# Kernel tuning notes

Measured on AMD Instinct MI355X. Metric: run time of the kernel, lower is better.

## Reference

```python
import jax, jax.numpy as jnp
import numpy as np

B, A, N = 1024, 64, 256   # batch, n_agent, obs_shape
M = 128                    # thought_size
H = M // 2                 # bi-LSTM hidden per direction
ACT = 64                   # action_shape
E_ATT = 64                 # attention embedding
E1 = M                     # actor_1 embedding (defaults to thought_size)
E2 = M                     # actor_2 embedding
K = 8                      # agent_per_group
THRESH = 0.5
LN_EPS = 1e-5


def setup_inputs() -> dict:
    key = jax.random.key(0)
    ks = jax.random.split(key, 32)
    r = lambda k, shp, s=0.05: jax.random.normal(k, shp, jnp.float32) * s
    return {
        'obs': jax.random.normal(ks[0], (B, A, N), jnp.float32),
        # actor_1: Linear(N,E1) -> LayerNorm(E1) -> ReLU -> Linear(E1,M)
        'a1_w1': r(ks[1], (E1, N)), 'a1_b1': r(ks[2], (E1,)),
        'ln_g': jnp.ones((E1,), jnp.float32), 'ln_b': jnp.zeros((E1,), jnp.float32),
        'a1_w2': r(ks[3], (M, E1)), 'a1_b2': r(ks[4], (M,)),
        # attention unit: 3-layer MLP
        'att_w1': r(ks[5], (E_ATT, M)), 'att_b1': r(ks[6], (E_ATT,)),
        'att_w2': r(ks[7], (E_ATT, E_ATT)), 'att_b2': r(ks[8], (E_ATT,)),
        'att_w3': r(ks[9], (1, E_ATT)), 'att_b3': r(ks[10], (1,)),
        # bi-LSTM (torch gate order i,f,g,o), forward + backward directions
        'wih_f': r(ks[11], (4 * H, M)), 'whh_f': r(ks[12], (4 * H, H)),
        'bih_f': r(ks[13], (4 * H,)), 'bhh_f': r(ks[14], (4 * H,)),
        'wih_b': r(ks[15], (4 * H, M)), 'whh_b': r(ks[16], (4 * H, H)),
        'bih_b': r(ks[17], (4 * H,)), 'bhh_b': r(ks[18], (4 * H,)),
        # actor_2: ReLU -> Linear(2M,E2) -> Linear(E2,ACT,no bias) -> Tanh
        'a2_w1': r(ks[19], (E2, 2 * M)), 'a2_b1': r(ks[20], (E2,)),
        'a2_w2': r(ks[21], (ACT, E2)),
    }


def _lstm_dir(x, wih, whh, b):
    # x: (T, M) single sequence; returns (T, H)
    def cell(carry, xt):
        h, c = carry
        z = xt @ wih.T + h @ whh.T + b
        i, f, g, o = jnp.split(z, 4)
        c = jax.nn.sigmoid(f) * c + jax.nn.sigmoid(i) * jnp.tanh(g)
        h = jax.nn.sigmoid(o) * jnp.tanh(c)
        return (h, c), h
    init = (jnp.zeros((H,), x.dtype), jnp.zeros((H,), x.dtype))
    _, hs = jax.lax.scan(cell, init, x)
    return hs


def _bilstm(x, wih_f, whh_f, bf, wih_b, whh_b, bb):
    hf = _lstm_dir(x, wih_f, whh_f, bf)
    hb = _lstm_dir(x[::-1], wih_b, whh_b, bb)[::-1]
    return jnp.concatenate([hf, hb], axis=-1)  # (T, 2H) == (T, M)


def reference(obs, a1_w1, a1_b1, ln_g, ln_b, a1_w2, a1_b2,
              att_w1, att_b1, att_w2, att_b2, att_w3, att_b3,
              wih_f, whh_f, bih_f, bhh_f, wih_b, whh_b, bih_b, bhh_b,
              a2_w1, a2_b1, a2_w2):
    # ---- actor_1: obs -> thoughts ----
    h = obs @ a1_w1.T + a1_b1
    mu = h.mean(-1, keepdims=True)
    var = ((h - mu) ** 2).mean(-1, keepdims=True)
    h = (h - mu) * jax.lax.rsqrt(var + LN_EPS) * ln_g + ln_b
    thoughts = jax.nn.relu(h) @ a1_w2.T + a1_b2  # (B, A, M)

    # ---- attention unit: initiator probability ----
    a = jax.nn.relu(thoughts @ att_w1.T + att_b1)
    a = jax.nn.relu(a @ att_w2.T + att_b2)
    init_prob = jax.nn.sigmoid((a @ att_w3.T + att_b3)[..., 0])  # (B, A)
    is_init = init_prob > THRESH

    # ---- group formation: K nearest agents by squared distance ----
    dot = jnp.einsum('bim,bjm->bij', thoughts, thoughts)
    sq = jnp.einsum('bim,bim->bi', thoughts, thoughts)
    dists = sq[:, None, :] - 2.0 * dot + sq[:, :, None]  # (B, A, A)
    # torch scatters by ascending agent index (j-loop), so sort chosen indices
    idx = jnp.sort(jnp.argsort(dists, axis=-1)[..., :K], axis=-1)  # (B, A, K)

    # ---- sequential gather -> bi-LSTM -> scatter, per initiator in order ----
    bf, bb = bih_f + bhh_f, bih_b + bhh_b

    def update_one_batch(nt0, idx_b, init_b):
        def body(nt, inp):
            idx_i, init_i = inp
            gathered = nt[idx_i]                      # (K, M) from CURRENT state
            integ = _bilstm(gathered, wih_f, whh_f, bf, wih_b, whh_b, bb)
            upd = nt.at[idx_i].set(integ)
            return jnp.where(init_i, upd, nt), None
        nt, _ = jax.lax.scan(body, nt0, (idx_b, init_b))
        return nt

    new_thoughts = jax.vmap(update_one_batch)(thoughts, idx, is_init)  # (B, A, M)

    # ---- actor_2 ----
    x = jax.nn.relu(jnp.concatenate([thoughts, new_thoughts], axis=-1))
    x = x @ a2_w1.T + a2_b1
    action = jnp.tanh(x @ a2_w2.T)  # (B, A, ACT)
    return action


if __name__ == '__main__':
    out = reference(**setup_inputs())
    print(out.shape)
```

## Files before the change

### kernel.cpp

```cpp
#include <hip/hip_runtime.h>

typedef unsigned int u32;
typedef unsigned short u16;
typedef unsigned long long u64;
typedef _Float16 h2 __attribute__((ext_vector_type(2)));
typedef _Float16 h4 __attribute__((ext_vector_type(4)));
typedef _Float16 h8 __attribute__((ext_vector_type(8)));
typedef float f4 __attribute__((ext_vector_type(4)));

#define ROWS 65536
#define NB 1024
#define NA 64

__device__ __forceinline__ float dot4(float4 w, float4 x){
  return w.x*x.x + w.y*x.y + w.z*x.z + w.w*x.w;
}
__device__ __forceinline__ h2 u32_h2(u32 v){ union { u32 u; h2 h; } x; x.u = v; return x.h; }
__device__ __forceinline__ h2 pack_h2(float a, float b){ h2 r; r.x = (_Float16)a; r.y = (_Float16)b; return r; }
__device__ __forceinline__ h4 pack_h4(float4 v){
  h4 r; r.x=(_Float16)v.x; r.y=(_Float16)v.y; r.z=(_Float16)v.z; r.w=(_Float16)v.w; return r;
}
__device__ __forceinline__ h4 pack_h4_relu(float4 v){
  h4 r; r.x=(_Float16)fmaxf(v.x,0.f); r.y=(_Float16)fmaxf(v.y,0.f);
  r.z=(_Float16)fmaxf(v.z,0.f); r.w=(_Float16)fmaxf(v.w,0.f); return r;
}
__device__ __forceinline__ float fsig(float z){
  float e = __builtin_amdgcn_exp2f(-1.44269504f * z);
  return __builtin_amdgcn_rcpf(1.0f + e);
}
__device__ __forceinline__ float ftanh(float z){
  float e = __builtin_amdgcn_exp2f(2.885390082f * z);
  return 1.0f - 2.0f * __builtin_amdgcn_rcpf(1.0f + e);
}
__device__ __forceinline__ h8 load8f(const float* p){
  float4 a = *(const float4*)p;
  float4 b = *(const float4*)(p + 4);
  h8 r;
  r[0] = (_Float16)a.x; r[1] = (_Float16)a.y; r[2] = (_Float16)a.z; r[3] = (_Float16)a.w;
  r[4] = (_Float16)b.x; r[5] = (_Float16)b.y; r[6] = (_Float16)b.z; r[7] = (_Float16)b.w;
  return r;
}

__global__ __launch_bounds__(256) void k_cvt(
    const float* __restrict__ a2w1, const float* __restrict__ a2w2,
    _Float16* __restrict__ w1h, _Float16* __restrict__ w2h)
{
  int i = blockIdx.x * 256 + threadIdx.x;
  if (i < 32768) w1h[i] = (_Float16)a2w1[i];
  if (i < 8192)  w2h[i] = (_Float16)a2w2[i];
}

__global__ __launch_bounds__(128) void k_actor1(
    const float* __restrict__ obs, const float* __restrict__ w1, const float* __restrict__ b1,
    const float* __restrict__ lng, const float* __restrict__ lnb,
    const float* __restrict__ w2, const float* __restrict__ b2,
    const float* __restrict__ aw1, const float* __restrict__ ab1,
    const float* __restrict__ aw2, const float* __restrict__ ab2,
    const float* __restrict__ aw3, const float* __restrict__ ab3,
    float* __restrict__ thoughts, int* __restrict__ isinit)
{
  const int b0 = blockIdx.x * 8;
  const int t = threadIdx.x;
  __shared__ float4 xs[8][64];
  __shared__ float hs[8][128];
  __shared__ float tb[8][128];
  __shared__ float ab[8][64];
  __shared__ float a2b[8][64];
  __shared__ float red[8][4];

  { const float4* og = (const float4*)(obs + (size_t)b0 * 256);
    #pragma unroll
    for (int j = 0; j < 4; j++){ int p = j * 128 + t; xs[p >> 6][p & 63] = og[p]; } }
  __syncthreads();

  float acc[8];
  #pragma unroll
  for (int r = 0; r < 8; r++) acc[r] = b1[t];
  { const float4* wr = (const float4*)(w1 + (size_t)t * 256);
    for (int j = 0; j < 64; j++){
      float4 w = wr[j];
      #pragma unroll
      for (int r = 0; r < 8; r++) acc[r] += dot4(w, xs[r][j]);
    } }

  #pragma unroll
  for (int r = 0; r < 8; r++){
    float s = acc[r], s2 = acc[r] * acc[r];
    #pragma unroll
    for (int off = 32; off > 0; off >>= 1){ s += __shfl_down(s, off); s2 += __shfl_down(s2, off); }
    if ((t & 63) == 0){ red[r][t >> 6] = s; red[r][2 + (t >> 6)] = s2; }
  }
  __syncthreads();
  const float g_ = lng[t], bb_ = lnb[t];
  #pragma unroll
  for (int r = 0; r < 8; r++){
    float mu  = (red[r][0] + red[r][1]) * (1.0f/128.0f);
    float var = (red[r][2] + red[r][3]) * (1.0f/128.0f) - mu * mu;
    hs[r][t] = fmaxf((acc[r] - mu) * rsqrtf(var + 1e-5f) * g_ + bb_, 0.0f);
  }
  __syncthreads();

  float acc2[8];
  #pragma unroll
  for (int r = 0; r < 8; r++) acc2[r] = b2[t];
  { const float4* wr = (const float4*)(w2 + (size_t)t * 128);
    for (int j = 0; j < 32; j++){
      float4 w = wr[j];
      #pragma unroll
      for (int r = 0; r < 8; r++) acc2[r] += dot4(w, ((const float4*)hs[r])[j]);
    } }
  #pragma unroll
  for (int r = 0; r < 8; r++){
    thoughts[(size_t)(b0 + r) * 128 + t] = acc2[r];
    tb[r][t] = acc2[r];
  }
  __syncthreads();

  if (t < 64){
    float a[8];
    #pragma unroll
    for (int r = 0; r < 8; r++) a[r] = ab1[t];
    const float4* wr = (const float4*)(aw1 + (size_t)t * 128);
    for (int j = 0; j < 32; j++){
      float4 w = wr[j];
      #pragma unroll
      for (int r = 0; r < 8; r++) a[r] += dot4(w, ((const float4*)tb[r])[j]);
    }
    #pragma unroll
    for (int r = 0; r < 8; r++) ab[r][t] = fmaxf(a[r], 0.0f);
  }
  __syncthreads();
  if (t < 64){
    float a[8];
    #pragma unroll
    for (int r = 0; r < 8; r++) a[r] = ab2[t];
    const float4* wr = (const float4*)(aw2 + (size_t)t * 64);
    for (int j = 0; j < 16; j++){
      float4 w = wr[j];
      #pragma unroll
      for (int r = 0; r < 8; r++) a[r] += dot4(w, ((const float4*)ab[r])[j]);
    }
    #pragma unroll
    for (int r = 0; r < 8; r++) a2b[r][t] = fmaxf(a[r], 0.0f);
  }
  __syncthreads();
  if (t < 8){
    float p = ab3[0];
    for (int j = 0; j < 64; j++) p += aw3[j] * a2b[t][j];
    isinit[b0 + t] = (p > 0.0f) ? 1 : 0;
  }
}

__global__ __launch_bounds__(256) void k_groups(
    const float* __restrict__ thoughts, int* __restrict__ idxout)
{
  const int b = blockIdx.x;
  const int tid = threadIdx.x;
  __shared__ float T[64 * 130];
  __shared__ float sq[64];
  for (int p = tid; p < 8192; p += 256){
    T[(p >> 7) * 130 + (p & 127)] = thoughts[(size_t)b * 8192 + p];
  }
  __syncthreads();
  if (tid < 64){
    const float2* tj = (const float2*)&T[tid * 130];
    float s = 0.0f;
    #pragma unroll 8
    for (int k = 0; k < 64; k++){ float2 v = tj[k]; s += v.x*v.x + v.y*v.y; }
    sq[tid] = s;
  }
  __syncthreads();
  const int lane = tid & 63;
  const int wv = tid >> 6;
  const float2* tj = (const float2*)&T[lane * 130];
  const float sqj = sq[lane];
  for (int ii = 0; ii < 16; ii++){
    const int i = wv * 16 + ii;
    const float2* ti = (const float2*)&T[i * 130];
    float dot = 0.0f;
    #pragma unroll 8
    for (int k = 0; k < 64; k++){ float2 a = ti[k]; float2 c = tj[k]; dot += a.x*c.x + a.y*c.y; }
    float d = fmaxf(sq[i] + sqj - 2.0f*dot, 0.0f);
    u64 key = (((u64)__float_as_uint(d)) << 32) | (u32)lane;
    u64 mask = 0;
    for (int q = 0; q < 8; q++){
      u64 m = key;
      #pragma unroll
      for (int off = 32; off > 0; off >>= 1){ u64 o = __shfl_xor(m, off); if (o < m) m = o; }
      mask |= 1ull << (u32)(m & 63u);
      if (key == m) key = ~0ull;
    }
    if (lane == 0){
      u64 mm = mask;
      int base = (b * 64 + i) * 8;
      #pragma unroll
      for (int q = 0; q < 8; q++){ int j = (int)__builtin_ctzll(mm); mm &= mm - 1; idxout[base + q] = j; }
    }
  }
}

__global__ __launch_bounds__(512) void k_scan(
    const float* __restrict__ thoughts, const int* __restrict__ isinit, const int* __restrict__ idx,
    const float* __restrict__ wihf, const float* __restrict__ whhf,
    const float* __restrict__ bihf, const float* __restrict__ bhhf,
    const float* __restrict__ wihb, const float* __restrict__ whhb,
    const float* __restrict__ bihb, const float* __restrict__ bhhb,
    float* __restrict__ newt)
{
  const int b    = blockIdx.x;
  const int tid  = threadIdx.x;
  const int w    = tid >> 6;
  const int lane = tid & 63;
  const int dir  = w >> 2;
  const int wsub = w & 3;
  const int lr   = lane & 15;
  const int hi   = lane >> 4;

  __shared__ __align__(16) _Float16 nt16[64 * 136];
  __shared__ __align__(16) _Float16 Zx16[2*8*64*4];
  __shared__ __align__(16) _Float16 hb16[2][64];
  __shared__ int gall[512];
  __shared__ int flags[64];
  __shared__ int dirty[64];

  const float* wih = dir ? wihb : wihf;
  const float* whh = dir ? whhb : whhf;

  h8 Bf[4][4];
  #pragma unroll
  for (int ni = 0; ni < 4; ni++){
    const float* wr = wih + (size_t)((wsub << 6) + (ni << 4) + lr) * 128 + (hi << 3);
    #pragma unroll
    for (int kt = 0; kt < 4; kt++) Bf[ni][kt] = load8f(wr + kt * 32);
    __builtin_amdgcn_sched_barrier(0);
  }
  h8 Bh[4][2];
  #pragma unroll
  for (int gg = 0; gg < 4; gg++){
    const float* wr = whh + (size_t)((gg << 6) + (wsub << 4) + lr) * 64 + (hi << 3);
    #pragma unroll
    for (int kt = 0; kt < 2; kt++) Bh[gg][kt] = load8f(wr + kt * 32);
    __builtin_amdgcn_sched_barrier(0);
  }
  float biasl[4];
  {
    const float* bih = dir ? bihb : bihf;
    const float* bhh = dir ? bhhb : bhhf;
    #pragma unroll
    for (int ni = 0; ni < 4; ni++){
      int n = (wsub << 6) + (ni << 4) + lr;
      biasl[ni] = bih[n] + bhh[n];
    }
  }

  { const float4* tf4 = (const float4*)(thoughts + (size_t)b * 8192);
    #pragma unroll
    for (int k2 = 0; k2 < 4; k2++){
      int id4 = tid + k2 * 512;
      float4 v = tf4[id4];
      *(h4*)&nt16[(id4 >> 5) * 136 + (id4 & 31) * 4] = pack_h4(v);
    } }
  gall[tid] = idx[(size_t)b * 512 + tid];
  if (tid < 64){ flags[tid] = isinit[b * 64 + tid]; dirty[tid] = 0; }
  __syncthreads();

  #pragma unroll 1
  for (int i = 0; i < 64; i++){
    if (!flags[i]) continue;
    if (tid < 8) dirty[gall[i * 8 + tid]] = 1;
    const int grow = gall[i * 8 + (lr & 7)];

    {
      h8 Af[4];
      #pragma unroll
      for (int kt = 0; kt < 4; kt++)
        Af[kt] = *(const h8*)&nt16[grow * 136 + kt * 32 + (hi << 3)];
      #pragma unroll
      for (int ni = 0; ni < 4; ni++){
        f4 acc = {0.0f, 0.0f, 0.0f, 0.0f};
        #pragma unroll
        for (int kt = 0; kt < 4; kt++)
          acc = __builtin_amdgcn_mfma_f32_16x16x32_f16(Af[kt], Bf[ni][kt], acc, 0, 0, 0);
        if (lane < 32){
          const int t0 = hi << 2, lp = (ni << 4) + lr;
          #pragma unroll
          for (int r = 0; r < 4; r++)
            Zx16[(((dir << 3) + t0 + r) * 64 + lp) * 4 + wsub] = (_Float16)(acc[r] + biasl[ni]);
        }
      }
    }
    __syncthreads();

    float c = 0.0f;
    #pragma unroll
    for (int s = 0; s < 8; s++){
      const int tt = dir ? (7 - s) : s;
      uint2 zr = *(const uint2*)&Zx16[(((dir << 3) + tt) * 64 + (wsub << 4) + lr) * 4];
      h2 zlo = u32_h2(zr.x), zhi2 = u32_h2(zr.y);
      float z0 = (float)zlo.x, z1 = (float)zlo.y, z2 = (float)zhi2.x, z3 = (float)zhi2.y;
      if (s > 0){
        h8 a0 = *(const h8*)&hb16[dir][(hi << 3)];
        h8 a1 = *(const h8*)&hb16[dir][32 + (hi << 3)];
        f4 A0 = {z0, 0.0f, 0.0f, 0.0f};
        f4 A1 = {z1, 0.0f, 0.0f, 0.0f};
        f4 A2 = {z2, 0.0f, 0.0f, 0.0f};
        f4 A3 = {z3, 0.0f, 0.0f, 0.0f};
        A0 = __builtin_amdgcn_mfma_f32_16x16x32_f16(a0, Bh[0][0], A0, 0, 0, 0);
        A0 = __builtin_amdgcn_mfma_f32_16x16x32_f16(a1, Bh[0][1], A0, 0, 0, 0);
        A1 = __builtin_amdgcn_mfma_f32_16x16x32_f16(a0, Bh[1][0], A1, 0, 0, 0);
        A1 = __builtin_amdgcn_mfma_f32_16x16x32_f16(a1, Bh[1][1], A1, 0, 0, 0);
        A2 = __builtin_amdgcn_mfma_f32_16x16x32_f16(a0, Bh[2][0], A2, 0, 0, 0);
        A2 = __builtin_amdgcn_mfma_f32_16x16x32_f16(a1, Bh[2][1], A2, 0, 0, 0);
        A3 = __builtin_amdgcn_mfma_f32_16x16x32_f16(a0, Bh[3][0], A3, 0, 0, 0);
        A3 = __builtin_amdgcn_mfma_f32_16x16x32_f16(a1, Bh[3][1], A3, 0, 0, 0);
        z0 = A0[0]; z1 = A1[0]; z2 = A2[0]; z3 = A3[0];
      }
      float fi = fsig(z0);
      float ff = fsig(z1);
      float fg = ftanh(z2);
      float fo = fsig(z3);
      c = ff * c + fi * fg;
      float hn = fo * ftanh(c);
      if (hi == 0){
        hb16[dir][(wsub << 4) + lr] = (_Float16)hn;
        int gt = gall[i * 8 + tt];
        nt16[gt * 136 + (dir << 6) + (wsub << 4) + lr] = (_Float16)hn;
      }
      __syncthreads();
    }
  }

  __syncthreads();
  { const float4* tf4 = (const float4*)(thoughts + (size_t)b * 8192);
    float4* of4 = (float4*)(newt + (size_t)b * 8192);
    #pragma unroll
    for (int k2 = 0; k2 < 4; k2++){
      int id4 = tid + k2 * 512;
      int row = id4 >> 5, c4 = (id4 & 31) * 4;
      float4 v = tf4[id4];
      if (dirty[row]){
        h4 hv = *(const h4*)&nt16[row * 136 + c4];
        v.x = (float)hv.x; v.y = (float)hv.y; v.z = (float)hv.z; v.w = (float)hv.w;
      }
      of4[id4] = v;
    } }
}

__global__ __launch_bounds__(256) void k_actor2(
    const float* __restrict__ thoughts, const float* __restrict__ newt,
    const _Float16* __restrict__ w1h, const float* __restrict__ b1,
    const _Float16* __restrict__ w2h, float* __restrict__ out)
{
  const int b0 = blockIdx.x * 32;
  const int tid = threadIdx.x;
  const int w = tid >> 6, lane = tid & 63, lr = lane & 15, hi = lane >> 4;
  const int mt = w & 1, nb = (w >> 1) << 6;

  __shared__ __align__(16) _Float16 Xc[32 * 264];
  __shared__ __align__(16) _Float16 Ys[32 * 136];

  #pragma unroll
  for (int k2 = 0; k2 < 8; k2++){
    int id4 = tid + k2 * 256;
    int row = id4 >> 6, c4 = (id4 & 63) * 4;
    const float* src = (c4 < 128) ? (thoughts + (size_t)(b0 + row) * 128 + c4)
                                  : (newt + (size_t)(b0 + row) * 128 + (c4 - 128));
    float4 v = *(const float4*)src;
    *(h4*)&Xc[row * 264 + c4] = pack_h4_relu(v);
  }
  __syncthreads();

  {
    h8 Af[8];
    #pragma unroll
    for (int kt = 0; kt < 8; kt++)
      Af[kt] = *(const h8*)&Xc[(mt * 16 + lr) * 264 + kt * 32 + (hi << 3)];
    #pragma unroll
    for (int ni = 0; ni < 4; ni++){
      const int n = nb + ni * 16 + lr;
      const _Float16* wr = w1h + (size_t)n * 256 + (hi << 3);
      f4 acc = {0.0f, 0.0f, 0.0f, 0.0f};
      #pragma unroll
      for (int kt = 0; kt < 8; kt++){
        h8 bfr = *(const h8*)(wr + kt * 32);
        acc = __builtin_amdgcn_mfma_f32_16x16x32_f16(Af[kt], bfr, acc, 0, 0, 0);
      }
      const float bb = b1[n];
      #pragma unroll
      for (int r = 0; r < 4; r++){
        int row = mt * 16 + (hi << 2) + r;
        Ys[row * 136 + n] = (_Float16)(acc[r] + bb);
      }
    }
  }
  __syncthreads();

  {
    const int ni0 = (w >> 1) << 1;
    h8 Ag[4];
    #pragma unroll
    for (int kt = 0; kt < 4; kt++)
      Ag[kt] = *(const h8*)&Ys[(mt * 16 + lr) * 136 + kt * 32 + (hi << 3)];
    #pragma unroll
    for (int nj = 0; nj < 2; nj++){
      const int n = (ni0 + nj) * 16 + lr;
      const _Float16* wr = w2h + (size_t)n * 128 + (hi << 3);
      f4 acc = {0.0f, 0.0f, 0.0f, 0.0f};
      #pragma unroll
      for (int kt = 0; kt < 4; kt++){
        h8 bfr = *(const h8*)(wr + kt * 32);
        acc = __builtin_amdgcn_mfma_f32_16x16x32_f16(Ag[kt], bfr, acc, 0, 0, 0);
      }
      #pragma unroll
      for (int r = 0; r < 4; r++){
        int row = mt * 16 + (hi << 2) + r;
        out[(size_t)(b0 + row) * 64 + n] = ftanh(acc[r]);
      }
    }
  }
}

extern "C" void kernel_launch(void* const* d_in, const int* in_sizes, int n_in,
                              void* d_out, int out_size, void* d_ws, size_t ws_size,
                              hipStream_t stream)
{
  const float* obs  = (const float*)d_in[0];
  const float* w1   = (const float*)d_in[1];
  const float* b1   = (const float*)d_in[2];
  const float* lng  = (const float*)d_in[3];
  const float* lnb  = (const float*)d_in[4];
  const float* w2   = (const float*)d_in[5];
  const float* b2   = (const float*)d_in[6];
  const float* aw1  = (const float*)d_in[7];
  const float* ab1  = (const float*)d_in[8];
  const float* aw2  = (const float*)d_in[9];
  const float* ab2  = (const float*)d_in[10];
  const float* aw3  = (const float*)d_in[11];
  const float* ab3  = (const float*)d_in[12];
  const float* wihf = (const float*)d_in[13];
  const float* whhf = (const float*)d_in[14];
  const float* bihf = (const float*)d_in[15];
  const float* bhhf = (const float*)d_in[16];
  const float* wihb = (const float*)d_in[17];
  const float* whhb = (const float*)d_in[18];
  const float* bihb = (const float*)d_in[19];
  const float* bhhb = (const float*)d_in[20];
  const float* a2w1 = (const float*)d_in[21];
  const float* a2b1 = (const float*)d_in[22];
  const float* a2w2 = (const float*)d_in[23];

  float* thoughts = (float*)d_ws;
  float* newt     = thoughts + (size_t)ROWS * 128;
  int*   isinit   = (int*)(newt + (size_t)ROWS * 128);
  int*   idxb     = isinit + ROWS;
  _Float16* w1h   = (_Float16*)(idxb + (size_t)ROWS * 8);
  _Float16* w2h   = w1h + 32768;

  hipLaunchKernelGGL(k_cvt, dim3(128), dim3(256), 0, stream, a2w1, a2w2, w1h, w2h);
  hipLaunchKernelGGL(k_actor1, dim3(ROWS / 8), dim3(128), 0, stream,
                     obs, w1, b1, lng, lnb, w2, b2, aw1, ab1, aw2, ab2, aw3, ab3,
                     thoughts, isinit);
  hipLaunchKernelGGL(k_groups, dim3(NB), dim3(256), 0, stream, thoughts, idxb);
  hipLaunchKernelGGL(k_scan, dim3(NB), dim3(512), 0, stream,
                     thoughts, isinit, idxb,
                     wihf, whhf, bihf, bhhf, wihb, whhb, bihb, bhhb, newt);
  hipLaunchKernelGGL(k_actor2, dim3(ROWS / 32), dim3(256), 0, stream,
                     thoughts, newt, w1h, a2b1, w2h, (float*)d_out);
}
```

Baseline: 1.011 ms.

## Run LSTM recurrence in one wave per direction using bpermute instead of block barriers

Restructures the bi-LSTM scan kernel so one wave per direction owns the whole recurrent step. It keeps all of W_hh in registers and broadcasts the hidden state across lanes with ds_bpermute, which removes the per-timestep block-wide __syncthreads and the shared-memory hidden-state buffer. The other three waves per direction take over the input projection, spread over 16 column tiles. The price is serial work concentrated in one wave, with 32 MFMAs per step instead of 8 per wave, 16 bpermutes per step, and high register pressure from 32 h8 weight fragments.

```diff
diff --git a/kernel.cpp b/kernel.cpp
--- a/kernel.cpp
+++ b/kernel.cpp
@@ -39,6 +39,9 @@
   r[0] = (_Float16)a.x; r[1] = (_Float16)a.y; r[2] = (_Float16)a.z; r[3] = (_Float16)a.w;
   r[4] = (_Float16)b.x; r[5] = (_Float16)b.y; r[6] = (_Float16)b.z; r[7] = (_Float16)b.w;
   return r;
+}
+__device__ __forceinline__ float bperm_f(int addr, float v){
+  return __int_as_float(__builtin_amdgcn_ds_bpermute(addr, __float_as_int(v)));
 }
 
 __global__ __launch_bounds__(256) void k_cvt(
@@ -215,10 +218,10 @@
   const int wsub = w & 3;
   const int lr   = lane & 15;
   const int hi   = lane >> 4;
+  const bool isB = (wsub == 0);
 
   __shared__ __align__(16) _Float16 nt16[64 * 136];
   __shared__ __align__(16) _Float16 Zx16[2*8*64*4];
-  __shared__ __align__(16) _Float16 hb16[2][64];
   __shared__ int gall[512];
   __shared__ int flags[64];
   __shared__ int dirty[64];
@@ -226,30 +229,32 @@
   const float* wih = dir ? wihb : wihf;
   const float* whh = dir ? whhb : whhf;
 
-  h8 Bf[4][4];
-  #pragma unroll
-  for (int ni = 0; ni < 4; ni++){
-    const float* wr = wih + (size_t)((wsub << 6) + (ni << 4) + lr) * 128 + (hi << 3);
-    #pragma unroll
-    for (int kt = 0; kt < 4; kt++) Bf[ni][kt] = load8f(wr + kt * 32);
-    __builtin_amdgcn_sched_barrier(0);
-  }
-  h8 Bh[4][2];
-  #pragma unroll
-  for (int gg = 0; gg < 4; gg++){
-    const float* wr = whh + (size_t)((gg << 6) + (wsub << 4) + lr) * 64 + (hi << 3);
-    #pragma unroll
-    for (int kt = 0; kt < 2; kt++) Bh[gg][kt] = load8f(wr + kt * 32);
-    __builtin_amdgcn_sched_barrier(0);
-  }
-  float biasl[4];
-  {
+  h8 W[32];
+  float biasl[6];
+  if (isB){
+    #pragma unroll
+    for (int ct = 0; ct < 16; ct++){
+      const int n = ((ct >> 2) << 6) + ((ct & 3) << 4) + lr;
+      const float* wr = whh + (size_t)n * 64 + (hi << 3);
+      W[ct * 2 + 0] = load8f(wr);
+      W[ct * 2 + 1] = load8f(wr + 32);
+      __builtin_amdgcn_sched_barrier(0);
+    }
+  } else {
+    const int ai = wsub - 1;
     const float* bih = dir ? bihb : bihf;
     const float* bhh = dir ? bhhb : bhhf;
     #pragma unroll
-    for (int ni = 0; ni < 4; ni++){
-      int n = (wsub << 6) + (ni << 4) + lr;
-      biasl[ni] = bih[n] + bhh[n];
+    for (int k = 0; k < 6; k++){
+      const int ct = ai * 6 + k;
+      if (ct < 16){
+        const int n = ((ct >> 2) << 6) + ((ct & 3) << 4) + lr;
+        const float* wr = wih + (size_t)n * 128 + (hi << 3);
+        #pragma unroll
+        for (int kt = 0; kt < 4; kt++) W[k * 4 + kt] = load8f(wr + kt * 32);
+        biasl[k] = bih[n] + bhh[n];
+      }
+      __builtin_amdgcn_sched_barrier(0);
     }
   }
 
@@ -268,66 +273,84 @@
   for (int i = 0; i < 64; i++){
     if (!flags[i]) continue;
     if (tid < 8) dirty[gall[i * 8 + tid]] = 1;
-    const int grow = gall[i * 8 + (lr & 7)];
-
-    {
+
+    if (!isB){
+      const int ai = wsub - 1;
+      const int grow = gall[i * 8 + (lr & 7)];
       h8 Af[4];
       #pragma unroll
       for (int kt = 0; kt < 4; kt++)
         Af[kt] = *(const h8*)&nt16[grow * 136 + kt * 32 + (hi << 3)];
       #pragma unroll
-      for (int ni = 0; ni < 4; ni++){
-        f4 acc = {0.0f, 0.0f, 0.0f, 0.0f};
-        #pragma unroll
-        for (int kt = 0; kt < 4; kt++)
-          acc = __builtin_amdgcn_mfma_f32_16x16x32_f16(Af[kt], Bf[ni][kt], acc, 0, 0, 0);
-        if (lane < 32){
-          const int t0 = hi << 2, lp = (ni << 4) + lr;
+      for (int k = 0; k < 6; k++){
+        const int ct = ai * 6 + k;
+        if (ct < 16){
+          f4 acc = {0.0f, 0.0f, 0.0f, 0.0f};
           #pragma unroll
-          for (int r = 0; r < 4; r++)
-            Zx16[(((dir << 3) + t0 + r) * 64 + lp) * 4 + wsub] = (_Float16)(acc[r] + biasl[ni]);
+          for (int kt = 0; kt < 4; kt++)
+            acc = __builtin_amdgcn_mfma_f32_16x16x32_f16(Af[kt], W[k * 4 + kt], acc, 0, 0, 0);
+          if (lane < 32){
+            const int t0 = hi << 2, lp = ((ct & 3) << 4) + lr, g = ct >> 2;
+            #pragma unroll
+            for (int r = 0; r < 4; r++)
+              Zx16[(((dir << 3) + t0 + r) * 64 + lp) * 4 + g] = (_Float16)(acc[r] + biasl[k]);
+          }
         }
       }
     }
     __syncthreads();
 
-    float c = 0.0f;
-    #pragma unroll
-    for (int s = 0; s < 8; s++){
-      const int tt = dir ? (7 - s) : s;
-      uint2 zr = *(const uint2*)&Zx16[(((dir << 3) + tt) * 64 + (wsub << 4) + lr) * 4];
-      h2 zlo = u32_h2(zr.x), zhi2 = u32_h2(zr.y);
-      float z0 = (float)zlo.x, z1 = (float)zlo.y, z2 = (float)zhi2.x, z3 = (float)zhi2.y;
-      if (s > 0){
-        h8 a0 = *(const h8*)&hb16[dir][(hi << 3)];
-        h8 a1 = *(const h8*)&hb16[dir][32 + (hi << 3)];
-        f4 A0 = {z0, 0.0f, 0.0f, 0.0f};
-        f4 A1 = {z1, 0.0f, 0.0f, 0.0f};
-        f4 A2 = {z2, 0.0f, 0.0f, 0.0f};
-        f4 A3 = {z3, 0.0f, 0.0f, 0.0f};
-        A0 = __builtin_amdgcn_mfma_f32_16x16x32_f16(a0, Bh[0][0], A0, 0, 0, 0);
-        A0 = __builtin_amdgcn_mfma_f32_16x16x32_f16(a1, Bh[0][1], A0, 0, 0, 0);
-        A1 = __builtin_amdgcn_mfma_f32_16x16x32_f16(a0, Bh[1][0], A1, 0, 0, 0);
-        A1 = __builtin_amdgcn_mfma_f32_16x16x32_f16(a1, Bh[1][1], A1, 0, 0, 0);
-        A2 = __builtin_amdgcn_mfma_f32_16x16x32_f16(a0, Bh[2][0], A2, 0, 0, 0);
-        A2 = __builtin_amdgcn_mfma_f32_16x16x32_f16(a1, Bh[2][1], A2, 0, 0, 0);
-        A3 = __builtin_amdgcn_mfma_f32_16x16x32_f16(a0, Bh[3][0], A3, 0, 0, 0);
-        A3 = __builtin_amdgcn_mfma_f32_16x16x32_f16(a1, Bh[3][1], A3, 0, 0, 0);
-        z0 = A0[0]; z1 = A1[0]; z2 = A2[0]; z3 = A3[0];
-      }
-      float fi = fsig(z0);
-      float ff = fsig(z1);
-      float fg = ftanh(z2);
-      float fo = fsig(z3);
-      c = ff * c + fi * fg;
-      float hn = fo * ftanh(c);
-      if (hi == 0){
-        hb16[dir][(wsub << 4) + lr] = (_Float16)hn;
-        int gt = gall[i * 8 + tt];
-        nt16[gt * 136 + (dir << 6) + (wsub << 4) + lr] = (_Float16)hn;
-      }
-      __syncthreads();
-    }
+    if (isB){
+      float c = 0.0f;
+      f4 acc[4][4];
+      #pragma unroll 1
+      for (int s = 0; s < 8; s++){
+        const int tt = dir ? (7 - s) : s;
+        uint2 zr = *(const uint2*)&Zx16[(((dir << 3) + tt) * 64 + lane) * 4];
+        h2 zlo = u32_h2(zr.x), zhi2 = u32_h2(zr.y);
+        float z0 = (float)zlo.x, z1 = (float)zlo.y, z2 = (float)zhi2.x, z3 = (float)zhi2.y;
+        if (s > 0){
+          z0 += (hi == 0 ? acc[0][0][0] : hi == 1 ? acc[0][1][0] : hi == 2 ? acc[0][2][0] : acc[0][3][0]);
+          z1 += (hi == 0 ? acc[1][0][0] : hi == 1 ? acc[1][1][0] : hi == 2 ? acc[1][2][0] : acc[1][3][0]);
+          z2 += (hi == 0 ? acc[2][0][0] : hi == 1 ? acc[2][1][0] : hi == 2 ? acc[2][2][0] : acc[2][3][0]);
+          z3 += (hi == 0 ? acc[3][0][0] : hi == 1 ? acc[3][1][0] : hi == 2 ? acc[3][2][0] : acc[3][3][0]);
+        }
+        float fi = fsig(z0);
+        float ff = fsig(z1);
+        float fg = ftanh(z2);
+        float fo = fsig(z3);
+        c = ff * c + fi * fg;
+        float hn = fo * ftanh(c);
+        nt16[gall[i * 8 + tt] * 136 + (dir << 6) + lane] = (_Float16)hn;
+        if (s < 7){
+          const int ab = hi << 5;
+          float p0 = bperm_f(ab +  0, hn), p1 = bperm_f(ab +  4, hn);
+          float p2 = bperm_f(ab +  8, hn), p3 = bperm_f(ab + 12, hn);
+          float p4 = bperm_f(ab + 16, hn), p5 = bperm_f(ab + 20, hn);
+          float p6 = bperm_f(ab + 24, hn), p7 = bperm_f(ab + 28, hn);
+          float q0 = bperm_f(ab + 128, hn), q1 = bperm_f(ab + 132, hn);
+          float q2 = bperm_f(ab + 136, hn), q3 = bperm_f(ab + 140, hn);
+          float q4 = bperm_f(ab + 144, hn), q5 = bperm_f(ab + 148, hn);
+          float q6 = bperm_f(ab + 152, hn), q7 = bperm_f(ab + 156, hn);
+          h8 a0, a1;
+          a0[0]=(_Float16)p0; a0[1]=(_Float16)p1; a0[2]=(_Float16)p2; a0[3]=(_Float16)p3;
+          a0[4]=(_Float16)p4; a0[5]=(_Float16)p5; a0[6]=(_Float16)p6; a0[7]=(_Float16)p7;
+          a1[0]=(_Float16)q0; a1[1]=(_Float16)q1; a1[2]=(_Float16)q2; a1[3]=(_Float16)q3;
+          a1[4]=(_Float16)q4; a1[5]=(_Float16)q5; a1[6]=(_Float16)q6; a1[7]=(_Float16)q7;
+          #pragma unroll
+          for (int g = 0; g < 4; g++){
+            #pragma unroll
+            for (int lt = 0; lt < 4; lt++){
+              f4 t = {0.0f, 0.0f, 0.0f, 0.0f};
+              t = __builtin_amdgcn_mfma_f32_16x16x32_f16(a0, W[(g * 4 + lt) * 2 + 0], t, 0, 0, 0);
+              t = __builtin_amdgcn_mfma_f32_16x16x32_f16(a1, W[(g * 4 + lt) * 2 + 1], t, 0, 0, 0);
+              acc[g][lt] = t;
+            }
+          }
+        }
+      }
+    }
+    __syncthreads();
   }
 
   __syncthreads();
```

New measurement: 1.390 ms. +37.5%, slower.

## Process two batches per scan block to fill MFMA rows and share syncs

Applied to the files above, without the earlier changes.

Each k_scan block now handles two batch elements. The input-projection MFMA uses all 16 rows, 8 agents from each batch, where it previously used only 8. The recurrent steps of both batches run interleaved between the same barriers. This halves the grid, amortises weight loading into registers and shares barrier overhead across two sequences. In exchange, LDS use per block doubles and there are fewer blocks, and a step runs whenever either batch is an initiator, so one batch's inactive steps are paid by the other.

```diff
diff --git a/kernel.cpp b/kernel.cpp
--- a/kernel.cpp
+++ b/kernel.cpp
@@ -207,7 +207,7 @@
     const float* __restrict__ bihb, const float* __restrict__ bhhb,
     float* __restrict__ newt)
 {
-  const int b    = blockIdx.x;
+  const int b0   = blockIdx.x * 2;
   const int tid  = threadIdx.x;
   const int w    = tid >> 6;
   const int lane = tid & 63;
@@ -216,12 +216,12 @@
   const int lr   = lane & 15;
   const int hi   = lane >> 4;
 
-  __shared__ __align__(16) _Float16 nt16[64 * 136];
-  __shared__ __align__(16) _Float16 Zx16[2*8*64*4];
-  __shared__ __align__(16) _Float16 hb16[2][64];
-  __shared__ int gall[512];
-  __shared__ int flags[64];
-  __shared__ int dirty[64];
+  __shared__ __align__(16) _Float16 nt16[2][64 * 136];
+  __shared__ __align__(16) _Float16 Zx16[2][2*8*64*4];
+  __shared__ __align__(16) _Float16 hb16[2][2][64];
+  __shared__ int gall[2][512];
+  __shared__ int flags[2][64];
+  __shared__ int dirty[2][64];
 
   const float* wih = dir ? wihb : wihf;
   const float* whh = dir ? whhb : whhf;
@@ -253,97 +253,116 @@
     }
   }
 
-  { const float4* tf4 = (const float4*)(thoughts + (size_t)b * 8192);
+  #pragma unroll
+  for (int q = 0; q < 2; q++){
+    const float4* tf4 = (const float4*)(thoughts + (size_t)(b0 + q) * 8192);
     #pragma unroll
     for (int k2 = 0; k2 < 4; k2++){
       int id4 = tid + k2 * 512;
       float4 v = tf4[id4];
-      *(h4*)&nt16[(id4 >> 5) * 136 + (id4 & 31) * 4] = pack_h4(v);
-    } }
-  gall[tid] = idx[(size_t)b * 512 + tid];
-  if (tid < 64){ flags[tid] = isinit[b * 64 + tid]; dirty[tid] = 0; }
+      *(h4*)&nt16[q][(id4 >> 5) * 136 + (id4 & 31) * 4] = pack_h4(v);
+    }
+  }
+  { int p = tid;              gall[0][p] = idx[(size_t)b0 * 512 + p]; }
+  { int p = tid + 512;        gall[1][p - 512] = idx[(size_t)b0 * 512 + p]; }
+  if (tid < 128){ int q = tid >> 6, j = tid & 63;
+    flags[q][j] = isinit[(b0 + q) * 64 + j]; dirty[q][j] = 0; }
   __syncthreads();
 
   #pragma unroll 1
   for (int i = 0; i < 64; i++){
-    if (!flags[i]) continue;
-    if (tid < 8) dirty[gall[i * 8 + tid]] = 1;
-    const int grow = gall[i * 8 + (lr & 7)];
+    const int f0 = flags[0][i], f1 = flags[1][i];
+    if (!(f0 | f1)) continue;
+    if (tid < 16){ int q = tid >> 3, j = tid & 7;
+      if (q ? f1 : f0) dirty[q][gall[q][i * 8 + j]] = 1; }
 
     {
+      const int qa = lr >> 3;
+      const int grow = gall[qa][i * 8 + (lr & 7)];
       h8 Af[4];
       #pragma unroll
       for (int kt = 0; kt < 4; kt++)
-        Af[kt] = *(const h8*)&nt16[grow * 136 + kt * 32 + (hi << 3)];
+        Af[kt] = *(const h8*)&nt16[qa][grow * 136 + kt * 32 + (hi << 3)];
+      const int qo = hi >> 1, t0 = (hi & 1) << 2;
       #pragma unroll
       for (int ni = 0; ni < 4; ni++){
         f4 acc = {0.0f, 0.0f, 0.0f, 0.0f};
         #pragma unroll
         for (int kt = 0; kt < 4; kt++)
           acc = __builtin_amdgcn_mfma_f32_16x16x32_f16(Af[kt], Bf[ni][kt], acc, 0, 0, 0);
-        if (lane < 32){
-          const int t0 = hi << 2, lp = (ni << 4) + lr;
-          #pragma unroll
-          for (int r = 0; r < 4; r++)
-            Zx16[(((dir << 3) + t0 + r) * 64 + lp) * 4 + wsub] = (_Float16)(acc[r] + biasl[ni]);
-        }
+        const int lp = (ni << 4) + lr;
+        #pragma unroll
+        for (int r = 0; r < 4; r++)
+          Zx16[qo][(((dir << 3) + t0 + r) * 64 + lp) * 4 + wsub] = (_Float16)(acc[r] + biasl[ni]);
       }
     }
     __syncthreads();
 
-    float c = 0.0f;
+    float c0 = 0.0f, c1 = 0.0f;
     #pragma unroll
     for (int s = 0; s < 8; s++){
       const int tt = dir ? (7 - s) : s;
-      uint2 zr = *(const uint2*)&Zx16[(((dir << 3) + tt) * 64 + (wsub << 4) + lr) * 4];
-      h2 zlo = u32_h2(zr.x), zhi2 = u32_h2(zr.y);
-      float z0 = (float)zlo.x, z1 = (float)zlo.y, z2 = (float)zhi2.x, z3 = (float)zhi2.y;
-      if (s > 0){
-        h8 a0 = *(const h8*)&hb16[dir][(hi << 3)];
-        h8 a1 = *(const h8*)&hb16[dir][32 + (hi << 3)];
-        f4 A0 = {z0, 0.0f, 0.0f, 0.0f};
-        f4 A1 = {z1, 0.0f, 0.0f, 0.0f};
-        f4 A2 = {z2, 0.0f, 0.0f, 0.0f};
-        f4 A3 = {z3, 0.0f, 0.0f, 0.0f};
-        A0 = __builtin_amdgcn_mfma_f32_16x16x32_f16(a0, Bh[0][0], A0, 0, 0, 0);
-        A0 = __builtin_amdgcn_mfma_f32_16x16x32_f16(a1, Bh[0][1], A0, 0, 0, 0);
-        A1 = __builtin_amdgcn_mfma_f32_16x16x32_f16(a0, Bh[1][0], A1, 0, 0, 0);
-        A1 = __builtin_amdgcn_mfma_f32_16x16x32_f16(a1, Bh[1][1], A1, 0, 0, 0);
-        A2 = __builtin_amdgcn_mfma_f32_16x16x32_f16(a0, Bh[2][0], A2, 0, 0, 0);
-        A2 = __builtin_amdgcn_mfma_f32_16x16x32_f16(a1, Bh[2][1], A2, 0, 0, 0);
-        A3 = __builtin_amdgcn_mfma_f32_16x16x32_f16(a0, Bh[3][0], A3, 0, 0, 0);
-        A3 = __builtin_amdgcn_mfma_f32_16x16x32_f16(a1, Bh[3][1], A3, 0, 0, 0);
-        z0 = A0[0]; z1 = A1[0]; z2 = A2[0]; z3 = A3[0];
-      }
-      float fi = fsig(z0);
-      float ff = fsig(z1);
-      float fg = ftanh(z2);
-      float fo = fsig(z3);
-      c = ff * c + fi * fg;
-      float hn = fo * ftanh(c);
-      if (hi == 0){
-        hb16[dir][(wsub << 4) + lr] = (_Float16)hn;
-        int gt = gall[i * 8 + tt];
-        nt16[gt * 136 + (dir << 6) + (wsub << 4) + lr] = (_Float16)hn;
+      #pragma unroll
+      for (int q = 0; q < 2; q++){
+        if (!(q ? f1 : f0)) continue;
+        uint2 zr = *(const uint2*)&Zx16[q][(((dir << 3) + tt) * 64 + (wsub << 4) + lr) * 4];
+        h2 zlo = u32_h2(zr.x), zhi2 = u32_h2(zr.y);
+        float z0 = (float)zlo.x, z1 = (float)zlo.y, z2 = (float)zhi2.x, z3 = (float)zhi2.y;
+        if (s > 0){
+          h8 a0 = *(const h8*)&hb16[q][dir][(hi << 3)];
+          h8 a1 = *(const h8*)&hb16[q][dir][32 + (hi << 3)];
+          f4 A;
+          A = (f4){z0, 0.f, 0.f, 0.f};
+          A = __builtin_amdgcn_mfma_f32_16x16x32_f16(a0, Bh[0][0], A, 0, 0, 0);
+          A = __builtin_amdgcn_mfma_f32_16x16x32_f16(a1, Bh[0][1], A, 0, 0, 0);
+          z0 = A[0];
+          A = (f4){z1, 0.f, 0.f, 0.f};
+          A = __builtin_amdgcn_mfma_f32_16x16x32_f16(a0, Bh[1][0], A, 0, 0, 0);
+          A = __builtin_amdgcn_mfma_f32_16x16x32_f16(a1, Bh[1][1], A, 0, 0, 0);
+          z1 = A[0];
+          A = (f4){z2, 0.f, 0.f, 0.f};
+          A = __builtin_amdgcn_mfma_f32_16x16x32_f16(a0, Bh[2][0], A, 0, 0, 0);
+          A = __builtin_amdgcn_mfma_f32_16x16x32_f16(a1, Bh[2][1], A, 0, 0, 0);
+          z2 = A[0];
+          A = (f4){z3, 0.f, 0.f, 0.f};
+          A = __builtin_amdgcn_mfma_f32_16x16x32_f16(a0, Bh[3][0], A, 0, 0, 0);
+          A = __builtin_amdgcn_mfma_f32_16x16x32_f16(a1, Bh[3][1], A, 0, 0, 0);
+          z3 = A[0];
+        }
+        float fi = fsig(z0);
+        float ff = fsig(z1);
+        float fg = ftanh(z2);
+        float fo = fsig(z3);
+        float cc = (q ? c1 : c0);
+        cc = ff * cc + fi * fg;
+        if (q) c1 = cc; else c0 = cc;
+        float hn = fo * ftanh(cc);
+        if (hi == 0){
+          hb16[q][dir][(wsub << 4) + lr] = (_Float16)hn;
+          nt16[q][gall[q][i * 8 + tt] * 136 + (dir << 6) + (wsub << 4) + lr] = (_Float16)hn;
+        }
       }
       __syncthreads();
     }
   }
 
   __syncthreads();
-  { const float4* tf4 = (const float4*)(thoughts + (size_t)b * 8192);
-    float4* of4 = (float4*)(newt + (size_t)b * 8192);
+  #pragma unroll
+  for (int q = 0; q < 2; q++){
+    const float4* tf4 = (const float4*)(thoughts + (size_t)(b0 + q) * 8192);
+    float4* of4 = (float4*)(newt + (size_t)(b0 + q) * 8192);
     #pragma unroll
     for (int k2 = 0; k2 < 4; k2++){
       int id4 = tid + k2 * 512;
       int row = id4 >> 5, c4 = (id4 & 31) * 4;
       float4 v = tf4[id4];
-      if (dirty[row]){
-        h4 hv = *(const h4*)&nt16[row * 136 + c4];
+      if (dirty[q][row]){
+        h4 hv = *(const h4*)&nt16[q][row * 136 + c4];
         v.x = (float)hv.x; v.y = (float)hv.y; v.z = (float)hv.z; v.w = (float)hv.w;
       }
       of4[id4] = v;
-    } }
+    }
+  }
 }
 
 __global__ __launch_bounds__(256) void k_actor2(
@@ -461,7 +480,7 @@
                      obs, w1, b1, lng, lnb, w2, b2, aw1, ab1, aw2, ab2, aw3, ab3,
                      thoughts, isinit);
   hipLaunchKernelGGL(k_groups, dim3(NB), dim3(256), 0, stream, thoughts, idxb);
-  hipLaunchKernelGGL(k_scan, dim3(NB), dim3(512), 0, stream,
+  hipLaunchKernelGGL(k_scan, dim3(NB / 2), dim3(512), 0, stream,
                      thoughts, isinit, idxb,
                      wihf, whhf, bihf, bhhf, wihb, whhb, bihb, bhhb, newt);
   hipLaunchKernelGGL(k_actor2, dim3(ROWS / 32), dim3(256), 0, stream,
```

New measurement: 955.7 us. -5.5%, faster.
